# Kernel tuning notes

Measured on AMD Instinct MI355X. Metric: run time of the kernel, lower is better.

## Reference

```python
import math
import jax, jax.numpy as jnp
import numpy as np

B, L, D, I, S, DTR, K, PH = 8, 2048, 512, 256, 8, 32, 3, 128


def setup_inputs() -> dict:
    key = jax.random.key(0)
    ks = jax.random.split(key, 12)
    def nrm(k, shape, s=0.02):
        return jax.random.normal(k, shape, jnp.float32) * s
    # dt_proj bias: inverse-softplus of exp(linspace(log 0.02, log 0.2))
    dt_init = np.exp(np.linspace(math.log(0.02), math.log(0.2), I))
    dt_b = np.log(np.expm1(dt_init)).astype(np.float32)
    A_log = np.log(np.tile(np.arange(1, S + 1, dtype=np.float32), (I, 1)))
    return dict(
        x=jax.random.normal(ks[0], (B, L, D), jnp.float32),
        position=jax.random.uniform(ks[1], (B, L, 6), jnp.float32),
        ln_in_w=jnp.ones(D, jnp.float32), ln_in_b=jnp.zeros(D, jnp.float32),
        pos_w1=nrm(ks[2], (PH, 6), 0.1), pos_b1=jnp.zeros(PH, jnp.float32),
        pos_w2=nrm(ks[3], (D, PH), 0.05), pos_b2=jnp.zeros(D, jnp.float32),
        scan_in_w=nrm(ks[4], (2, D, D)),
        scan_cx_w=nrm(ks[5], (2, I, 1, K), 0.2),
        scan_cz_w=nrm(ks[6], (2, I, 1, K), 0.2),
        scan_xp_w=nrm(ks[7], (2, DTR + 2 * S, I)),
        scan_dt_w=nrm(ks[8], (2, I, DTR)),
        scan_dt_b=jnp.tile(jnp.asarray(dt_b)[None], (2, 1)),
        scan_Alog=jnp.tile(jnp.asarray(A_log)[None], (2, 1, 1)),
        scan_Dp=jnp.ones((2, I), jnp.float32),
        scan_out_w=nrm(ks[9], (2, D, D)),  # zero-init in source; randomized for non-trivial testing
        mix_w=nrm(ks[10], (D, 3 * D)),
        ln_out_w=jnp.ones(D, jnp.float32), ln_out_b=jnp.zeros(D, jnp.float32),
    )


def _ln(x, w, b, eps=1e-6):
    m = x.mean(-1, keepdims=True)
    v = ((x - m) ** 2).mean(-1, keepdims=True)
    return (x - m) * jax.lax.rsqrt(v + eps) * w + b


def _dwconv_silu(x, w):
    # x: [B, L, C], w: [C, 1, K] depthwise conv1d, 'same' padding, then SiLU
    y = jax.lax.conv_general_dilated(
        jnp.swapaxes(x, 1, 2), w, (1,), ((K // 2, K // 2),),
        feature_group_count=w.shape[0], dimension_numbers=('NCH', 'OIH', 'NCH'))
    return jax.nn.silu(jnp.swapaxes(y, 1, 2))


def _selective_scan(x, in_w, cx_w, cz_w, xp_w, dt_w, dt_b, Alog, Dp, out_w):
    # ReferenceSelectiveScan1D.forward, x: [B, L, D]
    xb, zb = jnp.split(x @ in_w.T, 2, axis=-1)
    xb = _dwconv_silu(xb, cx_w)
    zb = _dwconv_silu(zb, cz_w)
    proj = xb @ xp_w.T  # [B, L, DTR + 2S]
    dt_raw, b_raw, c_raw = jnp.split(proj, [DTR, DTR + S], axis=-1)
    delta = jnp.clip(jax.nn.softplus(dt_raw @ dt_w.T + dt_b), 1e-4, 1.0)  # [B, L, I]
    bt = jnp.tanh(b_raw)  # [B, L, S]
    ct = jnp.tanh(c_raw)  # [B, L, S]
    a = jax.nn.softplus(Alog) + 1e-4  # [I, S]
    xs = (jnp.swapaxes(delta, 0, 1), jnp.swapaxes(bt, 0, 1),
          jnp.swapaxes(ct, 0, 1), jnp.swapaxes(xb, 0, 1))

    def step(state, inp):
        d_t, b_t, c_t, x_t = inp
        decay = jnp.clip(jnp.exp(-d_t[..., None] * a), 1e-4, 1.0)  # [B, I, S]
        state = decay * state + (1.0 - decay) * (b_t[:, None, :] * x_t[..., None])
        y = jnp.einsum('bis,bs->bi', state, c_t) + Dp * x_t
        return state, y

    state0 = jnp.zeros((x.shape[0], I, S), jnp.float32)
    _, ys = jax.lax.scan(step, state0, xs)  # ys: [L, B, I]
    y = jnp.swapaxes(ys, 0, 1)
    return jnp.concatenate([y, zb], -1) @ out_w.T


def reference(x, position, ln_in_w, ln_in_b, pos_w1, pos_b1, pos_w2, pos_b2,
              scan_in_w, scan_cx_w, scan_cz_w, scan_xp_w, scan_dt_w, scan_dt_b,
              scan_Alog, scan_Dp, scan_out_w, mix_w, ln_out_w, ln_out_b):
    pos = jax.nn.gelu(position @ pos_w1.T + pos_b1, approximate=False) @ pos_w2.T + pos_b2
    si = _ln(x, ln_in_w, ln_in_b) + pos
    params = lambda i: (scan_in_w[i], scan_cx_w[i], scan_cz_w[i], scan_xp_w[i],
                        scan_dt_w[i], scan_dt_b[i], scan_Alog[i], scan_Dp[i], scan_out_w[i])
    fwd = _selective_scan(si, *params(0))
    bwd = jnp.flip(_selective_scan(jnp.flip(si, 1), *params(1)), 1)
    mixed = jnp.concatenate([fwd, bwd, si], -1) @ mix_w.T
    return _ln(mixed, ln_out_w, ln_out_b)
```

## Files before the change

### kernel.cpp

```cpp
#include <hip/hip_runtime.h>
#include <hip/hip_bf16.h>

typedef __hip_bfloat16 bf16;
typedef __attribute__((ext_vector_type(8))) short short8;
typedef __attribute__((ext_vector_type(4))) float floatx4;

#define BBB 8
#define LL 2048
#define DDD 512
#define II 256
#define SS 8
#define MM (BBB*LL)
#define CHUNK 32
#define NCH (LL/CHUNK)

#define WS_SI    0l
#define WS_U0    16777216l
#define WS_U1    33554432l
#define WS_XZ    50331648l
#define WS_POS   50331648l
#define WS_H     67108864l
#define WS_P     50331648l
#define WS_Q     58720256l
#define WS_SINB  67108864l
#define WS_XBC   83886080l
#define WS_MIXED 83886080l
#define WS_DELTA 100663296l
#define WS_BTCT  117440512l
#define WS_INWB  121634816l
#define WS_MIXWB 122683392l
#define WS_PW2B  124256256l
#define WS_OWT   124387328l
#define WS_WP    125435904l
#define WS_WD    126484480l
#define WS_XPWB  126746624l
#define WS_A2    126763008l
#define WS_WXT   126779392l
#define WS_WZT   126785536l

__device__ __forceinline__ float b2f(unsigned short u) {
    return __uint_as_float(((unsigned)u) << 16);
}
__device__ __forceinline__ float bload(const bf16* p) {
    return b2f(*(const unsigned short*)p);
}
__device__ __forceinline__ void bstore(bf16* p, float v) {
    *p = __float2bfloat16(v);
}
__device__ __forceinline__ float softplus_f(float x) {
    return fmaxf(x, 0.f) + log1pf(expf(-fabsf(x)));
}
__device__ __forceinline__ float silu_f(float x) {
    return x / (1.f + expf(-x));
}
__device__ __forceinline__ void gl_lds16(const bf16* g, void* l) {
    __builtin_amdgcn_global_load_lds(
        (const __attribute__((address_space(1))) unsigned int*)g,
        (__attribute__((address_space(3))) unsigned int*)l, 16, 0, 0);
}
__device__ __forceinline__ void block_mean_rstd(float v0, float v1, float* red,
                                                float& mean, float& rstd) {
    float s = v0 + v1, q = v0*v0 + v1*v1;
    #pragma unroll
    for (int off = 32; off > 0; off >>= 1) {
        s += __shfl_down(s, off);
        q += __shfl_down(q, off);
    }
    int w = threadIdx.x >> 6, lane = threadIdx.x & 63;
    if (lane == 0) { red[w*2] = s; red[w*2+1] = q; }
    __syncthreads();
    if (threadIdx.x == 0) {
        float ts = 0.f, tq = 0.f;
        #pragma unroll
        for (int i = 0; i < 4; ++i) { ts += red[i*2]; tq += red[i*2+1]; }
        red[8] = ts; red[9] = tq;
    }
    __syncthreads();
    float ts = red[8], tq = red[9];
    mean = ts * (1.f/DDD);
    float var = tq * (1.f/DDD) - mean*mean;
    rstd = rsqrtf(var + 1e-6f);
}

__global__ __launch_bounds__(256) void k_f2b(const float* __restrict__ src,
                                             bf16* __restrict__ dst, int n) {
    int i = (blockIdx.x*256 + threadIdx.x) * 4;
    if (i >= n) return;
    float4 v = *(const float4*)(src + i);
    bf16 t[4] = {__float2bfloat16(v.x), __float2bfloat16(v.y),
                 __float2bfloat16(v.z), __float2bfloat16(v.w)};
    *(ushort4*)(dst + i) = *(ushort4*)t;
}

__global__ __launch_bounds__(256) void k_tow(const float* __restrict__ ow,
                                             bf16* __restrict__ owT) {
    long idx = (long)blockIdx.x*256 + threadIdx.x;
    long d = idx >> 18; long rem = idx & 262143;
    long k = rem >> 9, c = rem & 511;
    bstore(owT + idx, ow[d*262144 + c*512 + k]);
}

__global__ __launch_bounds__(256) void k_wd(const float* __restrict__ dtw,
                                            const float* __restrict__ xpw,
                                            bf16* __restrict__ Wd) {
    int d = blockIdx.y;
    int i = blockIdx.x;
    int j = threadIdx.x;
    const float* wr = dtw + (long)d*II*32 + i*32;
    const float* xp = xpw + (long)d*48*II;
    float acc = 0.f;
    #pragma unroll
    for (int k = 0; k < 32; ++k) acc = fmaf(wr[k], xp[k*II + j], acc);
    bstore(Wd + ((long)d*II + i)*II + j, acc);
}

__global__ __launch_bounds__(256) void k_xpw16(const float* __restrict__ xpw,
                                               bf16* __restrict__ xpwb) {
    int idx = blockIdx.x*256 + threadIdx.x;
    int d = idx >> 12, rem = idx & 4095;
    bstore(xpwb + idx, xpw[(long)d*48*II + 32*II + rem]);
}

__global__ __launch_bounds__(256) void k_aprep(const float* __restrict__ Alog,
                                               float* __restrict__ a2) {
    int idx = blockIdx.x*256 + threadIdx.x;
    float a = softplus_f(Alog[idx]) + 1e-4f;
    a2[idx] = -1.4426950408889634f * a;
}

__global__ __launch_bounds__(256) void k_wt(const float* __restrict__ cxw,
                                            const float* __restrict__ czw,
                                            float* __restrict__ wxT,
                                            float* __restrict__ wzT) {
    int idx = blockIdx.x*256 + threadIdx.x;
    if (idx >= 1536) return;
    int d = idx / 768, rem = idx % 768;
    int k = rem >> 8, i = rem & 255;
    int kk = d ? (2 - k) : k;
    wxT[idx] = cxw[d*768 + i*3 + kk];
    wzT[idx] = czw[d*768 + i*3 + kk];
}

__global__ __launch_bounds__(256) void k_h(const float* __restrict__ position,
                                           const float* __restrict__ pw1,
                                           const float* __restrict__ pb1,
                                           bf16* __restrict__ H) {
    long idx = (long)blockIdx.x*256 + threadIdx.x;
    long row = idx >> 7; int ph = idx & 127;
    const float* p = position + row*6;
    const float* w = pw1 + ph*6;
    float v = pb1[ph];
    #pragma unroll
    for (int j = 0; j < 6; ++j) v = fmaf(p[j], w[j], v);
    v = 0.5f * v * (1.f + erff(v * 0.70710678118654752440f));
    bstore(H + idx, v);
}

__global__ __launch_bounds__(256) void k_ln_add(const float* __restrict__ x,
                                                const bf16* __restrict__ posout,
                                                const float* __restrict__ lnw,
                                                const float* __restrict__ lnb,
                                                const float* __restrict__ pb2,
                                                bf16* __restrict__ si) {
    __shared__ float red[10];
    long row = blockIdx.x; int t = threadIdx.x;
    float v0 = x[row*DDD + t], v1 = x[row*DDD + t + 256];
    float mean, rstd;
    block_mean_rstd(v0, v1, red, mean, rstd);
    float p0 = bload(posout + row*DDD + t)       + pb2[t];
    float p1 = bload(posout + row*DDD + t + 256) + pb2[t + 256];
    bstore(si + row*DDD + t,       (v0-mean)*rstd*lnw[t]     + lnb[t]     + p0);
    bstore(si + row*DDD + t + 256, (v1-mean)*rstd*lnw[t+256] + lnb[t+256] + p1);
}

#define GEMM_COMPUTE(Sa, Sb)                                                      \
    do {                                                                          \
        _Pragma("unroll")                                                         \
        for (int kk = 0; kk < 2; ++kk) {                                          \
            const int sa_ = ((kk*4 + lq) ^ (lr & 7)) * 16;                        \
            short8 af[4], bfr[4];                                                 \
            _Pragma("unroll")                                                     \
            for (int mi = 0; mi < 4; ++mi)                                        \
                af[mi] = *(const short8*)((const char*)&Sa[wm*64 + mi*16 + lr][0] + sa_); \
            _Pragma("unroll")                                                     \
            for (int ni = 0; ni < 4; ++ni)                                        \
                bfr[ni] = *(const short8*)((const char*)&Sb[wn*64 + ni*16 + lr][0] + sa_); \
            _Pragma("unroll")                                                     \
            for (int mi = 0; mi < 4; ++mi)                                        \
                _Pragma("unroll")                                                 \
                for (int ni = 0; ni < 4; ++ni)                                    \
                    acc[mi][ni] = __builtin_amdgcn_mfma_f32_16x16x32_bf16(        \
                        af[mi], bfr[ni], acc[mi][ni], 0, 0, 0);                   \
        }                                                                         \
    } while (0)

template<typename TC, int EPI = 0>
__global__ __launch_bounds__(256)
void gemm_mfma(const bf16* __restrict__ A, long lda,
               const bf16* __restrict__ B, long ldb,
               TC* __restrict__ C, long ldc, int Kdim,
               const float* __restrict__ bias,
               long zA, long zB, long zC, long zbias) {
    __shared__ short As0[128][64], Bs0[128][64];
    __shared__ short As1[128][64], Bs1[128][64];
    const int tid = threadIdx.x;
    const int lane = tid & 63;
    const int wave = tid >> 6;
    const int wm = wave >> 1, wn = wave & 1;
    const int lr = lane & 15, lq = lane >> 4;
    A += (long)blockIdx.z * zA;
    B += (long)blockIdx.z * zB;
    C += (long)blockIdx.z * zC;
    const float* bp = bias ? bias + (long)blockIdx.z * zbias : nullptr;
    int nwg = gridDim.x * gridDim.y;
    int bid = blockIdx.y * gridDim.x + blockIdx.x;
    int wg = (bid & 7) * (nwg >> 3) + (bid >> 3);
    const long m0 = (long)(wg / gridDim.x) * 128;
    const long n0 = (long)(wg % gridDim.x) * 128;

    const bf16* gA[4]; const bf16* gB[4]; int off16[4];
    #pragma unroll
    for (int q = 0; q < 4; ++q) {
        int ch = q*256 + tid;
        int r = ch >> 3;
        int g = (ch & 7) ^ (r & 7);
        gA[q] = A + (m0 + r)*lda + g*8;
        gB[q] = B + (n0 + r)*ldb + g*8;
        off16[q] = (q*256 + wave*64) * 16;
    }
#define STAGE_G(Sa, Sb, k0)                                   \
    do {                                                      \
        _Pragma("unroll")                                     \
        for (int q = 0; q < 4; ++q) {                         \
            gl_lds16(gA[q] + (k0), (char*)(Sa) + off16[q]);   \
            gl_lds16(gB[q] + (k0), (char*)(Sb) + off16[q]);   \
        }                                                     \
    } while (0)

    floatx4 acc[4][4];
    #pragma unroll
    for (int i = 0; i < 4; ++i)
        #pragma unroll
        for (int j = 0; j < 4; ++j)
            acc[i][j] = (floatx4){0.f, 0.f, 0.f, 0.f};

    const int NT = Kdim >> 6;
    STAGE_G(As0, Bs0, 0);
    __syncthreads();
    for (int t = 0; t < NT; t += 2) {
        STAGE_G(As1, Bs1, (long)(t + 1) << 6);
        GEMM_COMPUTE(As0, Bs0);
        __syncthreads();
        if (t + 2 < NT) STAGE_G(As0, Bs0, (long)(t + 2) << 6);
        GEMM_COMPUTE(As1, Bs1);
        __syncthreads();
    }
#undef STAGE_G
    #pragma unroll
    for (int mi = 0; mi < 4; ++mi)
        #pragma unroll
        for (int ni = 0; ni < 4; ++ni)
            #pragma unroll
            for (int r = 0; r < 4; ++r) {
                long row = m0 + wm*64 + mi*16 + lq*4 + r;
                long col = n0 + wn*64 + ni*16 + lr;
                float v = acc[mi][ni][r];
                if (EPI == 1)
                    v = fminf(fmaxf(softplus_f(v + bp[col]), 1e-4f), 1.0f);
                if constexpr (sizeof(TC) == 2) bstore((bf16*)C + row*ldc + col, v);
                else ((float*)C)[row*ldc + col] = v;
            }
}

__global__ __launch_bounds__(256) void k_btct(const bf16* __restrict__ xbc,
                                              const bf16* __restrict__ xpwb,
                                              float* __restrict__ btct) {
    int d = blockIdx.y;
    int wave = threadIdx.x >> 6, lane = threadIdx.x & 63;
    long r0 = (long)blockIdx.x*64 + wave*16;
    int lr = lane & 15, lq = lane >> 4;
    const bf16* xb = xbc  + (long)d*MM*II;
    const bf16* wp = xpwb + (long)d*16*II;
    floatx4 acc = (floatx4){0.f, 0.f, 0.f, 0.f};
    #pragma unroll
    for (int k0 = 0; k0 < II; k0 += 32) {
        short8 af = *(const short8*)(xb + (r0 + lr)*II + k0 + lq*8);
        short8 bf = *(const short8*)(wp + lr*II + k0 + lq*8);
        acc = __builtin_amdgcn_mfma_f32_16x16x32_bf16(af, bf, acc, 0, 0, 0);
    }
    #pragma unroll
    for (int r = 0; r < 4; ++r) {
        long row = r0 + lq*4 + r;
        btct[((long)d*MM + row)*16 + lr] = tanhf(acc[r]);
    }
}

__global__ __launch_bounds__(256) void k_conv(const bf16* __restrict__ xz,
                                              const float* __restrict__ wxT,
                                              const float* __restrict__ wzT,
                                              bf16* __restrict__ xbc,
                                              bf16* __restrict__ u0,
                                              bf16* __restrict__ u1) {
    int d = blockIdx.y;
    long idx = (long)blockIdx.x*256 + threadIdx.x;
    long row = idx >> 5; int i = (int)(idx & 31) * 8;
    long l = row & (LL-1);
    const float* wxp = wxT + d*768 + i;
    const float* wzp = wzT + d*768 + i;
    float wxr[3][8], wzr[3][8];
    #pragma unroll
    for (int k = 0; k < 3; ++k) {
        *(float4*)&wxr[k][0] = *(const float4*)(wxp + k*256);
        *(float4*)&wxr[k][4] = *(const float4*)(wxp + k*256 + 4);
        *(float4*)&wzr[k][0] = *(const float4*)(wzp + k*256);
        *(float4*)&wzr[k][4] = *(const float4*)(wzp + k*256 + 4);
    }
    const bf16* base = xz + row*1024 + (long)d*512;
    short8 xr[3], zr[3];
    #pragma unroll
    for (int k = 0; k < 3; ++k) {
        bool ok = (l + k >= 1) && (l + k <= LL);
        if (ok) {
            xr[k] = *(const short8*)(base + (long)(k-1)*1024 + i);
            zr[k] = *(const short8*)(base + (long)(k-1)*1024 + 256 + i);
        } else {
            xr[k] = (short8){0,0,0,0,0,0,0,0};
            zr[k] = (short8){0,0,0,0,0,0,0,0};
        }
    }
    bf16 ox[8], oz[8];
    #pragma unroll
    for (int j = 0; j < 8; ++j) {
        float ax = 0.f, az = 0.f;
        #pragma unroll
        for (int k = 0; k < 3; ++k) {
            ax = fmaf(b2f((unsigned short)xr[k][j]), wxr[k][j], ax);
            az = fmaf(b2f((unsigned short)zr[k][j]), wzr[k][j], az);
        }
        ox[j] = __float2bfloat16(silu_f(ax));
        oz[j] = __float2bfloat16(silu_f(az));
    }
    *(short8*)(xbc + (long)d*MM*II + row*II + i) = *(short8*)ox;
    bf16* u = d ? u1 : u0;
    *(short8*)(u + row*512 + 256 + i) = *(short8*)oz;
}

__global__ __launch_bounds__(256)
void gemm_mix3(const bf16* __restrict__ A0, const bf16* __restrict__ A1,
               const bf16* __restrict__ A2,
               const bf16* __restrict__ B0, const bf16* __restrict__ B1,
               const bf16* __restrict__ B2, long ldb2,
               float* __restrict__ C) {
    __shared__ short As0[128][64], Bs0[128][64];
    __shared__ short As1[128][64], Bs1[128][64];
    const int tid = threadIdx.x;
    const int lane = tid & 63;
    const int wave = tid >> 6;
    const int wm = wave >> 1, wn = wave & 1;
    const int lr = lane & 15, lq = lane >> 4;
    int nwg = gridDim.x * gridDim.y;
    int bid = blockIdx.y * gridDim.x + blockIdx.x;
    int wg = (bid & 7) * (nwg >> 3) + (bid >> 3);
    const long m0 = (long)(wg / gridDim.x) * 128;
    const long n0 = (long)(wg % gridDim.x) * 128;

    long aoff[4], boffA[4], boffB[4]; int off16[4];
    #pragma unroll
    for (int q = 0; q < 4; ++q) {
        int ch = q*256 + tid;
        int r = ch >> 3;
        int g = (ch & 7) ^ (r & 7);
        aoff[q]  = (m0 + r)*512 + g*8;
        boffA[q] = (n0 + r)*512 + g*8;
        boffB[q] = (n0 + r)*ldb2 + g*8;
        off16[q] = (q*256 + wave*64) * 16;
    }
#define STAGE_M(Sa, Sb, t)                                                   \
    do {                                                                     \
        int seg_ = (t) >> 3;                                                 \
        long kc_ = ((long)(t) << 6) & 511;                                   \
        const bf16* Ap_ = (seg_ == 0) ? A0 : (seg_ == 1 ? A1 : A2);          \
        const bf16* Bp_ = (seg_ == 0) ? B0 : (seg_ == 1 ? B1 : B2);          \
        _Pragma("unroll")                                                    \
        for (int q = 0; q < 4; ++q) {                                        \
            gl_lds16(Ap_ + aoff[q] + kc_, (char*)(Sa) + off16[q]);           \
            gl_lds16(Bp_ + (seg_ < 2 ? boffA[q] : boffB[q]) + kc_,           \
                     (char*)(Sb) + off16[q]);                                \
        }                                                                    \
    } while (0)

    floatx4 acc[4][4];
    #pragma unroll
    for (int i = 0; i < 4; ++i)
        #pragma unroll
        for (int j = 0; j < 4; ++j)
            acc[i][j] = (floatx4){0.f, 0.f, 0.f, 0.f};

    STAGE_M(As0, Bs0, 0);
    __syncthreads();
    for (int t = 0; t < 24; t += 2) {
        STAGE_M(As1, Bs1, t + 1);
        GEMM_COMPUTE(As0, Bs0);
        __syncthreads();
        if (t + 2 < 24) STAGE_M(As0, Bs0, t + 2);
        GEMM_COMPUTE(As1, Bs1);
        __syncthreads();
    }
#undef STAGE_M
    #pragma unroll
    for (int mi = 0; mi < 4; ++mi)
        #pragma unroll
        for (int ni = 0; ni < 4; ++ni)
            #pragma unroll
            for (int r = 0; r < 4; ++r) {
                long row = m0 + wm*64 + mi*16 + lq*4 + r;
                long col = n0 + wn*64 + ni*16 + lr;
                C[row*512 + col] = acc[mi][ni][r];
            }
}

__global__ __launch_bounds__(256) void k_scan1(const bf16* __restrict__ delta,
                                               const float* __restrict__ btct,
                                               const bf16* __restrict__ xbc,
                                               const float* __restrict__ a2,
                                               float* __restrict__ P,
                                               float* __restrict__ Q) {
    __shared__ float bts[CHUNK][8];
    int z = blockIdx.y;
    int d = z >> 3, b = z & 7;
    int c = blockIdx.x;
    int i = threadIdx.x;
    {
        int tt = threadIdx.x >> 3, s = threadIdx.x & 7;
        int t = c*CHUNK + tt;
        long l = d ? (LL-1-t) : t;
        long row = (long)b*LL + l;
        bts[tt][s] = btct[(long)d*MM*16 + row*16 + s];
    }
    const float* ap = a2 + ((long)d*II + i)*8;
    float4 aA = *(const float4*)(ap);
    float4 aB = *(const float4*)(ap + 4);
    float a2r[8] = {aA.x, aA.y, aA.z, aA.w, aB.x, aB.y, aB.z, aB.w};
    __syncthreads();

    int t0 = c*CHUNK;
    long l0 = d ? (long)(LL-1-t0) : (long)t0;
    long row0 = (long)b*LL + l0;
    long step = (d ? -1l : 1l) * II;
    const bf16* pd = delta + (long)d*MM*II + row0*II + i;
    const bf16* px = xbc   + (long)d*MM*II + row0*II + i;

    float Pv[8], Qv[8];
    #pragma unroll
    for (int s = 0; s < 8; ++s) { Pv[s] = 1.f; Qv[s] = 0.f; }

    float dv = bload(pd), xv = bload(px);
    for (int tt = 0; tt < CHUNK; ++tt) {
        float dvn = 0.f, xvn = 0.f;
        if (tt + 1 < CHUNK) { dvn = bload(pd + step); xvn = bload(px + step); }
        pd += step; px += step;
        float4 b0 = *(const float4*)&bts[tt][0];
        float4 b1 = *(const float4*)&bts[tt][4];
        float btv[8] = {b0.x, b0.y, b0.z, b0.w, b1.x, b1.y, b1.z, b1.w};
        #pragma unroll
        for (int s = 0; s < 8; ++s) {
            float dec = __builtin_amdgcn_fmed3f(exp2f(dv*a2r[s]), 1e-4f, 1.0f);
            Pv[s] *= dec;
            Qv[s] = fmaf(dec, Qv[s], (1.f - dec)*btv[s]*xv);
        }
        dv = dvn; xv = xvn;
    }
    long o = ((long)z*NCH + c)*2048 + (long)i*8;
    *(floatx4*)(P + o)     = (floatx4){Pv[0], Pv[1], Pv[2], Pv[3]};
    *(floatx4*)(P + o + 4) = (floatx4){Pv[4], Pv[5], Pv[6], Pv[7]};
    *(floatx4*)(Q + o)     = (floatx4){Qv[0], Qv[1], Qv[2], Qv[3]};
    *(floatx4*)(Q + o + 4) = (floatx4){Qv[4], Qv[5], Qv[6], Qv[7]};
}

__global__ __launch_bounds__(256) void k_scan2(const float* __restrict__ P,
                                               const float* __restrict__ Q,
                                               float* __restrict__ sinb) {
    int d = blockIdx.y;
    long idx = (long)blockIdx.x*256 + threadIdx.x;
    int b = (int)(idx >> 11); int rem = (int)(idx & 2047);
    long base = ((long)(d*8 + b)*NCH)*2048 + rem;
    float st = 0.f;
    for (int c = 0; c < NCH; ++c) {
        long o = base + (long)c*2048;
        sinb[o] = st;
        st = fmaf(P[o], st, Q[o]);
    }
}

__global__ __launch_bounds__(256) void k_scan3(const bf16* __restrict__ delta,
                                               const float* __restrict__ btct,
                                               const bf16* __restrict__ xbc,
                                               const float* __restrict__ a2,
                                               const float* __restrict__ Dp,
                                               const float* __restrict__ sinb,
                                               bf16* __restrict__ u0,
                                               bf16* __restrict__ u1) {
    __shared__ float bcs[CHUNK][16];
    int z = blockIdx.y;
    int d = z >> 3, b = z & 7;
    int c = blockIdx.x;
    int i = threadIdx.x;
    {
        int tt = threadIdx.x >> 3, col = (threadIdx.x & 7)*2;
        int t = c*CHUNK + tt;
        long l = d ? (LL-1-t) : t;
        long row = (long)b*LL + l;
        *(float2*)&bcs[tt][col] =
            *(const float2*)(btct + (long)d*MM*16 + row*16 + col);
    }
    const float* ap = a2 + ((long)d*II + i)*8;
    float4 aA = *(const float4*)(ap);
    float4 aB = *(const float4*)(ap + 4);
    float a2r[8] = {aA.x, aA.y, aA.z, aA.w, aB.x, aB.y, aB.z, aB.w};
    float dpv = Dp[d*II + i];
    const float* sb = sinb + ((long)z*NCH + c)*2048 + (long)i*8;
    float4 s0 = *(const float4*)(sb);
    float4 s1 = *(const float4*)(sb + 4);
    float st[8] = {s0.x, s0.y, s0.z, s0.w, s1.x, s1.y, s1.z, s1.w};
    __syncthreads();

    int t0 = c*CHUNK;
    long l0 = d ? (long)(LL-1-t0) : (long)t0;
    long row0 = (long)b*LL + l0;
    long step = (d ? -1l : 1l) * II;
    long ustep = (d ? -1l : 1l) * 512;
    const bf16* pd = delta + (long)d*MM*II + row0*II + i;
    const bf16* px = xbc   + (long)d*MM*II + row0*II + i;
    bf16* pu = (d ? u1 : u0) + row0*512 + i;

    float dv = bload(pd), xv = bload(px);
    for (int tt = 0; tt < CHUNK; ++tt) {
        float dvn = 0.f, xvn = 0.f;
        if (tt + 1 < CHUNK) { dvn = bload(pd + step); xvn = bload(px + step); }
        pd += step; px += step;
        const float4* q4 = (const float4*)&bcs[tt][0];
        float4 b0 = q4[0], b1 = q4[1], c0 = q4[2], c1 = q4[3];
        float btv[8] = {b0.x, b0.y, b0.z, b0.w, b1.x, b1.y, b1.z, b1.w};
        float ctv[8] = {c0.x, c0.y, c0.z, c0.w, c1.x, c1.y, c1.z, c1.w};
        float pa = dpv * xv;
        #pragma unroll
        for (int s = 0; s < 8; ++s) {
            float dec = __builtin_amdgcn_fmed3f(exp2f(dv*a2r[s]), 1e-4f, 1.0f);
            st[s] = fmaf(dec, st[s], (1.f - dec)*btv[s]*xv);
            pa = fmaf(st[s], ctv[s], pa);
        }
        bstore(pu, pa);
        pu += ustep;
        dv = dvn; xv = xvn;
    }
}

__global__ __launch_bounds__(256) void k_ln_out(const float* __restrict__ mixed,
                                                const float* __restrict__ w,
                                                const float* __restrict__ b,
                                                float* __restrict__ out) {
    __shared__ float red[10];
    long row = blockIdx.x; int t = threadIdx.x;
    float v0 = mixed[row*DDD + t], v1 = mixed[row*DDD + t + 256];
    float mean, rstd;
    block_mean_rstd(v0, v1, red, mean, rstd);
    out[row*DDD + t]       = (v0-mean)*rstd*w[t]     + b[t];
    out[row*DDD + t + 256] = (v1-mean)*rstd*w[t+256] + b[t+256];
}

extern "C" void kernel_launch(void* const* d_in, const int* in_sizes, int n_in,
                              void* d_out, int out_size, void* d_ws, size_t ws_size,
                              hipStream_t stream) {
    const float* x        = (const float*)d_in[0];
    const float* position = (const float*)d_in[1];
    const float* ln_in_w  = (const float*)d_in[2];
    const float* ln_in_b  = (const float*)d_in[3];
    const float* pos_w1   = (const float*)d_in[4];
    const float* pos_b1   = (const float*)d_in[5];
    const float* pos_w2   = (const float*)d_in[6];
    const float* pos_b2   = (const float*)d_in[7];
    const float* in_w     = (const float*)d_in[8];
    const float* cx_w     = (const float*)d_in[9];
    const float* cz_w     = (const float*)d_in[10];
    const float* xp_w     = (const float*)d_in[11];
    const float* dt_w     = (const float*)d_in[12];
    const float* dt_b     = (const float*)d_in[13];
    const float* Alog     = (const float*)d_in[14];
    const float* Dp       = (const float*)d_in[15];
    const float* out_w    = (const float*)d_in[16];
    const float* mix_w    = (const float*)d_in[17];
    const float* ln_out_w = (const float*)d_in[18];
    const float* ln_out_b = (const float*)d_in[19];
    float* out = (float*)d_out;

    char* base = (char*)d_ws;
    bf16*  si     = (bf16*)(base + WS_SI);
    bf16*  u0     = (bf16*)(base + WS_U0);
    bf16*  u1     = (bf16*)(base + WS_U1);
    bf16*  xz     = (bf16*)(base + WS_XZ);
    bf16*  posout = (bf16*)(base + WS_POS);
    bf16*  H      = (bf16*)(base + WS_H);
    float* Pb     = (float*)(base + WS_P);
    float* Qb     = (float*)(base + WS_Q);
    float* sinb   = (float*)(base + WS_SINB);
    bf16*  xbc    = (bf16*)(base + WS_XBC);
    bf16*  delta  = (bf16*)(base + WS_DELTA);
    float* btct   = (float*)(base + WS_BTCT);
    float* mixed  = (float*)(base + WS_MIXED);
    bf16*  in_wb  = (bf16*)(base + WS_INWB);
    bf16*  mix_wb = (bf16*)(base + WS_MIXWB);
    bf16*  pw2b   = (bf16*)(base + WS_PW2B);
    bf16*  owT    = (bf16*)(base + WS_OWT);
    bf16*  Wp     = (bf16*)(base + WS_WP);
    bf16*  Wd     = (bf16*)(base + WS_WD);
    bf16*  xpwb   = (bf16*)(base + WS_XPWB);
    float* a2     = (float*)(base + WS_A2);
    float* wxT    = (float*)(base + WS_WXT);
    float* wzT    = (float*)(base + WS_WZT);

    k_f2b<<<(524288/4+255)/256, 256, 0, stream>>>(in_w,  in_wb,  524288);
    k_f2b<<<(786432/4+255)/256, 256, 0, stream>>>(mix_w, mix_wb, 786432);
    k_f2b<<<(65536/4+255)/256, 256, 0, stream>>>(pos_w2, pw2b, 65536);
    k_tow<<<(524288+255)/256, 256, 0, stream>>>(out_w, owT);
    k_wd<<<dim3(256, 2), 256, 0, stream>>>(dt_w, xp_w, Wd);
    k_xpw16<<<32, 256, 0, stream>>>(xp_w, xpwb);
    k_aprep<<<16, 256, 0, stream>>>(Alog, a2);
    k_wt<<<6, 256, 0, stream>>>(cx_w, cz_w, wxT, wzT);
    gemm_mfma<bf16><<<dim3(4, 4, 2), 256, 0, stream>>>(
        mix_wb, 1536, owT, 512, Wp, 512, 512, nullptr, 512, 262144, 262144, 0);
    k_h<<<(MM*128)/256, 256, 0, stream>>>(position, pos_w1, pos_b1, H);
    gemm_mfma<bf16><<<dim3(4, MM/128), 256, 0, stream>>>(
        H, 128, pw2b, 128, posout, 512, 128, nullptr, 0, 0, 0, 0);
    k_ln_add<<<MM, 256, 0, stream>>>(x, posout, ln_in_w, ln_in_b, pos_b2, si);
    gemm_mfma<bf16><<<dim3(8, MM/128), 256, 0, stream>>>(
        si, 512, in_wb, 512, xz, 1024, 512, nullptr, 0, 0, 0, 0);
    k_conv<<<dim3((MM*32)/256, 2), 256, 0, stream>>>(xz, wxT, wzT, xbc, u0, u1);
    gemm_mfma<bf16, 1><<<dim3(2, MM/128, 2), 256, 0, stream>>>(
        xbc, 256, Wd, 256, delta, 256, 256, dt_b,
        (long)MM*II, 65536, (long)MM*II, 256);
    k_btct<<<dim3(MM/64, 2), 256, 0, stream>>>(xbc, xpwb, btct);
    k_scan1<<<dim3(NCH, 16), 256, 0, stream>>>(delta, btct, xbc, a2, Pb, Qb);
    k_scan2<<<dim3(64, 2), 256, 0, stream>>>(Pb, Qb, sinb);
    k_scan3<<<dim3(NCH, 16), 256, 0, stream>>>(delta, btct, xbc, a2, Dp,
                                               sinb, u0, u1);
    gemm_mix3<<<dim3(4, MM/128), 256, 0, stream>>>(u0, u1, si,
                                                   Wp, Wp + 262144, mix_wb + 1024, 1536,
                                                   mixed);
    k_ln_out<<<MM, 256, 0, stream>>>(mixed, ln_out_w, ln_out_b, out);
}
```

Baseline: 360.9 us.

## Fuse prep kernels into one launch, register-tile conv rows, store mixed as bf16

Nine small weight-prep and positional-hidden kernels are merged into a single launch that dispatches on block index, cutting launch overhead. The depthwise conv now has each thread produce four consecutive rows, so the neighbouring input rows it loads are shared instead of re-read per row. The mix GEMM writes its output in bf16 rather than fp32, halving traffic into the output layernorm at the cost of precision before normalization.

```diff
diff --git a/kernel.cpp b/kernel.cpp
--- a/kernel.cpp
+++ b/kernel.cpp
@@ -82,78 +82,81 @@
     rstd = rsqrtf(var + 1e-6f);
 }
 
-__global__ __launch_bounds__(256) void k_f2b(const float* __restrict__ src,
-                                             bf16* __restrict__ dst, int n) {
-    int i = (blockIdx.x*256 + threadIdx.x) * 4;
-    if (i >= n) return;
-    float4 v = *(const float4*)(src + i);
-    bf16 t[4] = {__float2bfloat16(v.x), __float2bfloat16(v.y),
-                 __float2bfloat16(v.z), __float2bfloat16(v.w)};
-    *(ushort4*)(dst + i) = *(ushort4*)t;
-}
-
-__global__ __launch_bounds__(256) void k_tow(const float* __restrict__ ow,
-                                             bf16* __restrict__ owT) {
-    long idx = (long)blockIdx.x*256 + threadIdx.x;
-    long d = idx >> 18; long rem = idx & 262143;
-    long k = rem >> 9, c = rem & 511;
-    bstore(owT + idx, ow[d*262144 + c*512 + k]);
-}
-
-__global__ __launch_bounds__(256) void k_wd(const float* __restrict__ dtw,
-                                            const float* __restrict__ xpw,
-                                            bf16* __restrict__ Wd) {
-    int d = blockIdx.y;
-    int i = blockIdx.x;
-    int j = threadIdx.x;
-    const float* wr = dtw + (long)d*II*32 + i*32;
-    const float* xp = xpw + (long)d*48*II;
-    float acc = 0.f;
-    #pragma unroll
-    for (int k = 0; k < 32; ++k) acc = fmaf(wr[k], xp[k*II + j], acc);
-    bstore(Wd + ((long)d*II + i)*II + j, acc);
-}
-
-__global__ __launch_bounds__(256) void k_xpw16(const float* __restrict__ xpw,
-                                               bf16* __restrict__ xpwb) {
-    int idx = blockIdx.x*256 + threadIdx.x;
-    int d = idx >> 12, rem = idx & 4095;
-    bstore(xpwb + idx, xpw[(long)d*48*II + 32*II + rem]);
-}
-
-__global__ __launch_bounds__(256) void k_aprep(const float* __restrict__ Alog,
-                                               float* __restrict__ a2) {
-    int idx = blockIdx.x*256 + threadIdx.x;
-    float a = softplus_f(Alog[idx]) + 1e-4f;
-    a2[idx] = -1.4426950408889634f * a;
-}
-
-__global__ __launch_bounds__(256) void k_wt(const float* __restrict__ cxw,
-                                            const float* __restrict__ czw,
-                                            float* __restrict__ wxT,
-                                            float* __restrict__ wzT) {
-    int idx = blockIdx.x*256 + threadIdx.x;
-    if (idx >= 1536) return;
-    int d = idx / 768, rem = idx % 768;
-    int k = rem >> 8, i = rem & 255;
-    int kk = d ? (2 - k) : k;
-    wxT[idx] = cxw[d*768 + i*3 + kk];
-    wzT[idx] = czw[d*768 + i*3 + kk];
-}
-
-__global__ __launch_bounds__(256) void k_h(const float* __restrict__ position,
-                                           const float* __restrict__ pw1,
-                                           const float* __restrict__ pb1,
-                                           bf16* __restrict__ H) {
-    long idx = (long)blockIdx.x*256 + threadIdx.x;
-    long row = idx >> 7; int ph = idx & 127;
-    const float* p = position + row*6;
-    const float* w = pw1 + ph*6;
-    float v = pb1[ph];
-    #pragma unroll
-    for (int j = 0; j < 6; ++j) v = fmaf(p[j], w[j], v);
-    v = 0.5f * v * (1.f + erff(v * 0.70710678118654752440f));
-    bstore(H + idx, v);
+__global__ __launch_bounds__(256)
+void k_prep(const float* __restrict__ position, const float* __restrict__ pw1,
+            const float* __restrict__ pb1, bf16* __restrict__ H,
+            const float* __restrict__ ow, bf16* __restrict__ owT,
+            const float* __restrict__ mixw, bf16* __restrict__ mixwb,
+            const float* __restrict__ inw, bf16* __restrict__ inwb,
+            const float* __restrict__ dtw, const float* __restrict__ xpw,
+            bf16* __restrict__ Wd,
+            const float* __restrict__ posw2, bf16* __restrict__ pw2b,
+            bf16* __restrict__ xpwb,
+            const float* __restrict__ Alog, float* __restrict__ a2,
+            const float* __restrict__ cxw, const float* __restrict__ czw,
+            float* __restrict__ wxT, float* __restrict__ wzT) {
+    int bb = blockIdx.x;
+    int tid = threadIdx.x;
+    if (bb < 8192) {
+        long idx = (long)bb*256 + tid;
+        long row = idx >> 7; int ph = idx & 127;
+        const float* p = position + row*6;
+        const float* w = pw1 + ph*6;
+        float v = pb1[ph];
+        #pragma unroll
+        for (int j = 0; j < 6; ++j) v = fmaf(p[j], w[j], v);
+        v = 0.5f * v * (1.f + erff(v * 0.70710678118654752440f));
+        bstore(H + idx, v);
+    } else if (bb < 10240) {
+        long idx = (long)(bb - 8192)*256 + tid;
+        long d = idx >> 18; long rem = idx & 262143;
+        long k = rem >> 9, c = rem & 511;
+        bstore(owT + idx, ow[d*262144 + c*512 + k]);
+    } else if (bb < 11008) {
+        int i = (bb - 10240)*256*4 + tid*4;
+        float4 v = *(const float4*)(mixw + i);
+        bf16 t[4] = {__float2bfloat16(v.x), __float2bfloat16(v.y),
+                     __float2bfloat16(v.z), __float2bfloat16(v.w)};
+        *(ushort4*)(mixwb + i) = *(ushort4*)t;
+    } else if (bb < 11520) {
+        int i = (bb - 11008)*256*4 + tid*4;
+        float4 v = *(const float4*)(inw + i);
+        bf16 t[4] = {__float2bfloat16(v.x), __float2bfloat16(v.y),
+                     __float2bfloat16(v.z), __float2bfloat16(v.w)};
+        *(ushort4*)(inwb + i) = *(ushort4*)t;
+    } else if (bb < 12032) {
+        int local = bb - 11520;
+        int d = local >> 8, i = local & 255, j = tid;
+        const float* wr = dtw + (long)d*II*32 + i*32;
+        const float* xp = xpw + (long)d*48*II;
+        float acc = 0.f;
+        #pragma unroll
+        for (int k = 0; k < 32; ++k) acc = fmaf(wr[k], xp[k*II + j], acc);
+        bstore(Wd + ((long)d*II + i)*II + j, acc);
+    } else if (bb < 12096) {
+        int i = (bb - 12032)*256*4 + tid*4;
+        float4 v = *(const float4*)(posw2 + i);
+        bf16 t[4] = {__float2bfloat16(v.x), __float2bfloat16(v.y),
+                     __float2bfloat16(v.z), __float2bfloat16(v.w)};
+        *(ushort4*)(pw2b + i) = *(ushort4*)t;
+    } else if (bb < 12128) {
+        int idx = (bb - 12096)*256 + tid;
+        int d = idx >> 12, rem = idx & 4095;
+        bstore(xpwb + idx, xpw[(long)d*48*II + 32*II + rem]);
+    } else if (bb < 12144) {
+        int idx = (bb - 12128)*256 + tid;
+        float a = softplus_f(Alog[idx]) + 1e-4f;
+        a2[idx] = -1.4426950408889634f * a;
+    } else {
+        int idx = (bb - 12144)*256 + tid;
+        if (idx < 1536) {
+            int d = idx / 768, rem = idx % 768;
+            int k = rem >> 8, i = rem & 255;
+            int kk = d ? (2 - k) : k;
+            wxT[idx] = cxw[d*768 + i*3 + kk];
+            wzT[idx] = czw[d*768 + i*3 + kk];
+        }
+    }
 }
 
 __global__ __launch_bounds__(256) void k_ln_add(const float* __restrict__ x,
@@ -303,8 +306,9 @@
                                               bf16* __restrict__ u1) {
     int d = blockIdx.y;
     long idx = (long)blockIdx.x*256 + threadIdx.x;
-    long row = idx >> 5; int i = (int)(idx & 31) * 8;
-    long l = row & (LL-1);
+    long rg = idx >> 5; int i = (int)(idx & 31) * 8;
+    long row0 = rg << 2;
+    int l0 = (int)(row0 & (LL-1));
     const float* wxp = wxT + d*768 + i;
     const float* wzp = wzT + d*768 + i;
     float wxr[3][8], wzr[3][8];
@@ -315,34 +319,38 @@
         *(float4*)&wzr[k][0] = *(const float4*)(wzp + k*256);
         *(float4*)&wzr[k][4] = *(const float4*)(wzp + k*256 + 4);
     }
-    const bf16* base = xz + row*1024 + (long)d*512;
-    short8 xr[3], zr[3];
-    #pragma unroll
-    for (int k = 0; k < 3; ++k) {
-        bool ok = (l + k >= 1) && (l + k <= LL);
+    const bf16* base = xz + row0*1024 + (long)d*512 + i;
+    short8 X[6], Z[6];
+    #pragma unroll
+    for (int k = 0; k < 6; ++k) {
+        int gl = l0 - 1 + k;
+        bool ok = (gl >= 0) && (gl < LL);
         if (ok) {
-            xr[k] = *(const short8*)(base + (long)(k-1)*1024 + i);
-            zr[k] = *(const short8*)(base + (long)(k-1)*1024 + 256 + i);
+            X[k] = *(const short8*)(base + (long)(k-1)*1024);
+            Z[k] = *(const short8*)(base + (long)(k-1)*1024 + 256);
         } else {
-            xr[k] = (short8){0,0,0,0,0,0,0,0};
-            zr[k] = (short8){0,0,0,0,0,0,0,0};
+            X[k] = (short8){0,0,0,0,0,0,0,0};
+            Z[k] = (short8){0,0,0,0,0,0,0,0};
         }
     }
-    bf16 ox[8], oz[8];
-    #pragma unroll
-    for (int j = 0; j < 8; ++j) {
-        float ax = 0.f, az = 0.f;
-        #pragma unroll
-        for (int k = 0; k < 3; ++k) {
-            ax = fmaf(b2f((unsigned short)xr[k][j]), wxr[k][j], ax);
-            az = fmaf(b2f((unsigned short)zr[k][j]), wzr[k][j], az);
+    bf16* u = d ? u1 : u0;
+    #pragma unroll
+    for (int r = 0; r < 4; ++r) {
+        bf16 ox[8], oz[8];
+        #pragma unroll
+        for (int j = 0; j < 8; ++j) {
+            float ax = 0.f, az = 0.f;
+            #pragma unroll
+            for (int k = 0; k < 3; ++k) {
+                ax = fmaf(b2f((unsigned short)X[r+k][j]), wxr[k][j], ax);
+                az = fmaf(b2f((unsigned short)Z[r+k][j]), wzr[k][j], az);
+            }
+            ox[j] = __float2bfloat16(silu_f(ax));
+            oz[j] = __float2bfloat16(silu_f(az));
         }
-        ox[j] = __float2bfloat16(silu_f(ax));
-        oz[j] = __float2bfloat16(silu_f(az));
-    }
-    *(short8*)(xbc + (long)d*MM*II + row*II + i) = *(short8*)ox;
-    bf16* u = d ? u1 : u0;
-    *(short8*)(u + row*512 + 256 + i) = *(short8*)oz;
+        *(short8*)(xbc + (long)d*MM*II + (row0+r)*II + i) = *(short8*)ox;
+        *(short8*)(u + (row0+r)*512 + 256 + i) = *(short8*)oz;
+    }
 }
 
 __global__ __launch_bounds__(256)
@@ -350,7 +358,7 @@
                const bf16* __restrict__ A2,
                const bf16* __restrict__ B0, const bf16* __restrict__ B1,
                const bf16* __restrict__ B2, long ldb2,
-               float* __restrict__ C) {
+               bf16* __restrict__ C) {
     __shared__ short As0[128][64], Bs0[128][64];
     __shared__ short As1[128][64], Bs1[128][64];
     const int tid = threadIdx.x;
@@ -415,7 +423,7 @@
             for (int r = 0; r < 4; ++r) {
                 long row = m0 + wm*64 + mi*16 + lq*4 + r;
                 long col = n0 + wn*64 + ni*16 + lr;
-                C[row*512 + col] = acc[mi][ni][r];
+                bstore(C + row*512 + col, acc[mi][ni][r]);
             }
 }
 
@@ -555,13 +563,13 @@
     }
 }
 
-__global__ __launch_bounds__(256) void k_ln_out(const float* __restrict__ mixed,
+__global__ __launch_bounds__(256) void k_ln_out(const bf16* __restrict__ mixed,
                                                 const float* __restrict__ w,
                                                 const float* __restrict__ b,
                                                 float* __restrict__ out) {
     __shared__ float red[10];
     long row = blockIdx.x; int t = threadIdx.x;
-    float v0 = mixed[row*DDD + t], v1 = mixed[row*DDD + t + 256];
+    float v0 = bload(mixed + row*DDD + t), v1 = bload(mixed + row*DDD + t + 256);
     float mean, rstd;
     block_mean_rstd(v0, v1, red, mean, rstd);
     out[row*DDD + t]       = (v0-mean)*rstd*w[t]     + b[t];
@@ -606,7 +614,7 @@
     bf16*  xbc    = (bf16*)(base + WS_XBC);
     bf16*  delta  = (bf16*)(base + WS_DELTA);
     float* btct   = (float*)(base + WS_BTCT);
-    float* mixed  = (float*)(base + WS_MIXED);
+    bf16*  mixed  = (bf16*)(base + WS_MIXED);
     bf16*  in_wb  = (bf16*)(base + WS_INWB);
     bf16*  mix_wb = (bf16*)(base + WS_MIXWB);
     bf16*  pw2b   = (bf16*)(base + WS_PW2B);
@@ -618,23 +626,18 @@
     float* wxT    = (float*)(base + WS_WXT);
     float* wzT    = (float*)(base + WS_WZT);
 
-    k_f2b<<<(524288/4+255)/256, 256, 0, stream>>>(in_w,  in_wb,  524288);
-    k_f2b<<<(786432/4+255)/256, 256, 0, stream>>>(mix_w, mix_wb, 786432);
-    k_f2b<<<(65536/4+255)/256, 256, 0, stream>>>(pos_w2, pw2b, 65536);
-    k_tow<<<(524288+255)/256, 256, 0, stream>>>(out_w, owT);
-    k_wd<<<dim3(256, 2), 256, 0, stream>>>(dt_w, xp_w, Wd);
-    k_xpw16<<<32, 256, 0, stream>>>(xp_w, xpwb);
-    k_aprep<<<16, 256, 0, stream>>>(Alog, a2);
-    k_wt<<<6, 256, 0, stream>>>(cx_w, cz_w, wxT, wzT);
+    k_prep<<<12150, 256, 0, stream>>>(position, pos_w1, pos_b1, H,
+                                      out_w, owT, mix_w, mix_wb, in_w, in_wb,
+                                      dt_w, xp_w, Wd, pos_w2, pw2b, xpwb,
+                                      Alog, a2, cx_w, cz_w, wxT, wzT);
     gemm_mfma<bf16><<<dim3(4, 4, 2), 256, 0, stream>>>(
         mix_wb, 1536, owT, 512, Wp, 512, 512, nullptr, 512, 262144, 262144, 0);
-    k_h<<<(MM*128)/256, 256, 0, stream>>>(position, pos_w1, pos_b1, H);
     gemm_mfma<bf16><<<dim3(4, MM/128), 256, 0, stream>>>(
         H, 128, pw2b, 128, posout, 512, 128, nullptr, 0, 0, 0, 0);
     k_ln_add<<<MM, 256, 0, stream>>>(x, posout, ln_in_w, ln_in_b, pos_b2, si);
     gemm_mfma<bf16><<<dim3(8, MM/128), 256, 0, stream>>>(
         si, 512, in_wb, 512, xz, 1024, 512, nullptr, 0, 0, 0, 0);
-    k_conv<<<dim3((MM*32)/256, 2), 256, 0, stream>>>(xz, wxT, wzT, xbc, u0, u1);
+    k_conv<<<dim3(512, 2), 256, 0, stream>>>(xz, wxT, wzT, xbc, u0, u1);
     gemm_mfma<bf16, 1><<<dim3(2, MM/128, 2), 256, 0, stream>>>(
         xbc, 256, Wd, 256, delta, 256, 256, dt_b,
         (long)MM*II, 65536, (long)MM*II, 256);
```

Result: no change. 356.4 us (-1.2%).
